# Performance work log

Hardware: AMD Instinct MI355X
Metric: run time of the kernel (lower is better)

Reference implementation:

```python
import jax, jax.numpy as jnp
import numpy as np

B, CTX, EMB = 4, 1024, 64
K, HID, NH = 8, 256, 8
GADD, NADD = 2, 2
RANK = 2                      # diags expand (..., k, 2) -> rank-2 index tuples
NPTS = K * (2 ** RANK + GADD + NADD)   # 64 points per token
SIGMA_BOOST = 2.0
EPS = 1e-6


def setup_inputs() -> dict:
    key = jax.random.key(0)
    ks = jax.random.split(key, 8)
    g = lambda k, shape, s: jax.random.normal(k, shape, jnp.float32) * s
    return {
        "x": g(ks[0], (B, CTX, EMB), 1.0),
        "Wq": g(ks[1], (EMB, EMB * NH), EMB ** -0.5),
        "Wk": g(ks[2], (EMB, EMB * NH), EMB ** -0.5),
        "Wv": g(ks[3], (EMB, EMB * NH), EMB ** -0.5),
        "Wu": g(ks[4], (EMB * NH, EMB), (EMB * NH) ** -0.5),
        "bu": jnp.zeros((EMB,), jnp.float32),
        "Wp1": g(ks[5], (EMB, HID), EMB ** -0.5),
        "bp1": jnp.zeros((HID,), jnp.float32),
        "Wp2": g(ks[6], (HID, 2 * K), HID ** -0.5),
        "bp2": jnp.zeros((2 * K,), jnp.float32),
        "mvalues": jnp.ones((CTX,), jnp.float32),
    }


def _forward(x, Wq, Wk, Wv, Wu, bu, Wp1, bp1, Wp2, bp2, mvalues):
    b, n, e = x.shape
    # ---- hyper network: per-token Gaussian mixture params ----
    h = jax.nn.relu(x @ Wp1 + bp1)
    params = h @ Wp2 + bp2                              # (b,n,2k)
    raw_means = params[:, :, :K][..., None]             # (b,n,k,1)
    raw_sigmas = params[:, :, K:]                       # (b,n,k)
    diags = jnp.arange(n, dtype=x.dtype)[None, :, None, None]
    means = jnp.broadcast_to(diags - jax.nn.softplus(raw_means), (b, n, K, RANK))
    means = jnp.clip(means, 0.0, n - 1.0)               # transform_means (clamp into range)
    sigmas = (jax.nn.softplus(raw_sigmas + SIGMA_BOOST) + EPS)[..., None]
    sigmas = jnp.broadcast_to(sigmas, (b, n, K, RANK))  # transform_sigmas

    # ---- ngenerate: 2^rank corners + global + local integer samples ----
    skey = jax.random.key(42)
    kg, kl = jax.random.split(skey)
    fl = jnp.floor(means).astype(jnp.int32)             # (b,n,k,2)
    offs = jnp.array([[0, 0], [0, 1], [1, 0], [1, 1]], jnp.int32)
    corners = fl[:, :, :, None, :] + offs               # (b,n,k,4,2)
    glob = jax.random.randint(kg, (b, n, K, GADD, RANK), 0, n)
    loc = fl[:, :, :, None, :] - 1 + jax.random.randint(kl, (b, n, K, NADD, RANK), 0, 2)
    idx = jnp.concatenate([corners, glob, loc], axis=3)
    idx = jnp.clip(idx, 0, n - 1).reshape(b, n, NPTS, RANK)

    # ---- nduplicates: mark repeat index tuples within each token ----
    eq = (idx[:, :, :, None, :] == idx[:, :, None, :, :]).all(-1)   # (b,n,p,p)
    tri = jnp.tril(jnp.ones((NPTS, NPTS), bool), -1)
    dup = (eq & tri).any(-1)                            # (b,n,p)

    # ---- densities: unnormalized Gaussians, zero dups, normalize over points ----
    pf = idx.astype(x.dtype)
    diff = (pf[:, :, :, None, :] - means[:, :, None, :, :]) / sigmas[:, :, None, :, :]
    dens = jnp.exp(-0.5 * (diff * diff).sum(-1))        # (b,n,p,k)
    dens = jnp.where(dup[..., None], 0.0, dens)
    dens = dens / dens.sum(axis=2, keepdims=True)
    weights = (mvalues[None, :, None, None] * dens).sum(-1)        # (b,n,p)

    # ---- heads ----
    BH = b * NH
    def heads(W):
        return (x @ W).reshape(b, n, NH, e).transpose(0, 2, 1, 3).reshape(BH, n, e)
    q = heads(Wq) / e ** 0.25
    k_ = heads(Wk) / e ** 0.25
    v = heads(Wv)

    P = n * NPTS
    idxh = jnp.broadcast_to(idx[:, None], (b, NH, n, NPTS, RANK)).reshape(BH, P, RANK)
    w = jnp.broadcast_to(weights[:, None], (b, NH, n, NPTS)).reshape(BH, P)
    rows, cols = idxh[..., 0], idxh[..., 1]

    # ---- gather q/k at sampled (row,col), per-element dot ----
    sq = jnp.take_along_axis(q, rows[:, :, None], axis=1)           # (BH,P,e)
    sk = jnp.take_along_axis(k_, cols[:, :, None], axis=1)
    dot = w * (sq * sk).sum(-1)                                     # (BH,P)

    # ---- sparse log-softmax over rows (stable, segment ops) ----
    seg = (jnp.arange(BH, dtype=jnp.int32)[:, None] * n + rows).reshape(-1)
    vflat = dot.reshape(-1)
    mx = jax.ops.segment_max(vflat, seg, num_segments=BH * n)
    ex = jnp.exp(vflat - mx[seg])
    Z = jax.ops.segment_sum(ex, seg, num_segments=BH * n)
    p = jnp.exp(vflat - (mx[seg] + jnp.log(Z[seg])))                # softmax probs

    # ---- sparse batchmm: scatter p * values[col] into rows ----
    sv = jnp.take_along_axis(v, cols[:, :, None], axis=1).reshape(-1, e)
    out = jax.ops.segment_sum(sv * p[:, None], seg, num_segments=BH * n)
    out = out.reshape(b, NH, n, e).transpose(0, 2, 1, 3).reshape(b, n, NH * e)
    return out @ Wu + bu


def reference(x, Wq, Wk, Wv, Wu, bu, Wp1, bp1, Wp2, bp2, mvalues):
    return _forward(x, Wq, Wk, Wv, Wu, bu, Wp1, bp1, Wp2, bp2, mvalues)
```

## Files before the change

kernel.cpp:

```cpp
#include <hip/hip_runtime.h>
#include <hip/hip_fp16.h>
#include <cstdint>
#include <cstddef>

#define BB 4
#define NN 1024
#define EMB_ 64
#define NH_ 8
#define BH_ (BB*NH_)
#define HID_ 256
#define K_ 8
#define NPTS_ 64
#define QB 512

__host__ __device__ inline void tf2x32(uint32_t k0, uint32_t k1, uint32_t c0, uint32_t c1,
                                       uint32_t &o0, uint32_t &o1) {
  uint32_t ks2 = k0 ^ k1 ^ 0x1BD11BDAu;
  uint32_t x0 = c0 + k0, x1 = c1 + k1;
#define TFR(r) { x0 += x1; x1 = (x1 << (r)) | (x1 >> (32 - (r))); x1 ^= x0; }
  TFR(13) TFR(15) TFR(26) TFR(6)
  x0 += k1;  x1 += ks2 + 1u;
  TFR(17) TFR(29) TFR(16) TFR(24)
  x0 += ks2; x1 += k0 + 2u;
  TFR(13) TFR(15) TFR(26) TFR(6)
  x0 += k0;  x1 += k1 + 3u;
  TFR(17) TFR(29) TFR(16) TFR(24)
  x0 += k1;  x1 += ks2 + 4u;
  TFR(13) TFR(15) TFR(26) TFR(6)
  x0 += ks2; x1 += k0 + 5u;
#undef TFR
  o0 = x0; o1 = x1;
}

__device__ inline uint32_t tf_bits(uint32_t k0, uint32_t k1, uint32_t idx) {
  uint32_t a, b;
  tf2x32(k0, k1, 0u, idx, a, b);
  return a ^ b;
}

__device__ inline float softplusf(float v) {
  return fmaxf(v, 0.f) + log1pf(expf(-fabsf(v)));
}

#define ROWS1 8
__global__ void __launch_bounds__(256) pre_kernel(
    const float* __restrict__ x,
    const float* __restrict__ Wq, const float* __restrict__ Wk, const float* __restrict__ Wv,
    const float* __restrict__ Wp1, const float* __restrict__ bp1,
    const float* __restrict__ Wp2, const float* __restrict__ bp2,
    const float* __restrict__ mvalues,
    float* __restrict__ q, __half* __restrict__ k, __half* __restrict__ v,
    int* __restrict__ prc, float* __restrict__ pw, int* __restrict__ counts,
    uint32_t kg0, uint32_t kg1, uint32_t kl0, uint32_t kl1) {
  __shared__ float xq[ROWS1][EMB_];
  __shared__ float xs[4][EMB_];
  __shared__ float hs[4][HID_];
  __shared__ float ps[4][16];
  __shared__ float meanv[4][K_], invsig[4][K_];
  __shared__ int flv[4][K_];
  __shared__ int pk[4][NPTS_];

  if (blockIdx.x < QB) {
    const int block0 = blockIdx.x * ROWS1;
    const int t = threadIdx.x;
    for (int i = t; i < ROWS1 * EMB_; i += 256) xq[i / EMB_][i % EMB_] = x[(size_t)block0 * EMB_ + i];
    __syncthreads();
    const float qkscale = 0.3535533905932738f;

    auto dmatf = [&](const float* __restrict__ W, float* __restrict__ o, float sc) {
      for (int half = 0; half < 2; half++) {
        const int c = half * 256 + t;
        float acc[ROWS1];
#pragma unroll
        for (int r = 0; r < ROWS1; r++) acc[r] = 0.f;
#pragma unroll 1
        for (int i4 = 0; i4 < EMB_; i4 += 4) {
          const float w0 = W[(i4 + 0) * 512 + c];
          const float w1 = W[(i4 + 1) * 512 + c];
          const float w2 = W[(i4 + 2) * 512 + c];
          const float w3 = W[(i4 + 3) * 512 + c];
#pragma unroll
          for (int r = 0; r < ROWS1; r++) {
            const float4 xv = *(const float4*)&xq[r][i4];
            acc[r] += xv.x * w0 + xv.y * w1 + xv.z * w2 + xv.w * w3;
          }
        }
        const int h = c >> 6, j = c & 63;
#pragma unroll
        for (int r = 0; r < ROWS1; r++) {
          const int gr = block0 + r;
          const int b = gr >> 10, n = gr & 1023;
          o[(((size_t)(b * NH_ + h) * NN + n)) * EMB_ + j] = acc[r] * sc;
        }
      }
    };
    auto dmath = [&](const float* __restrict__ W, __half* __restrict__ o, float sc) {
      for (int half = 0; half < 2; half++) {
        const int c = half * 256 + t;
        float acc[ROWS1];
#pragma unroll
        for (int r = 0; r < ROWS1; r++) acc[r] = 0.f;
#pragma unroll 1
        for (int i4 = 0; i4 < EMB_; i4 += 4) {
          const float w0 = W[(i4 + 0) * 512 + c];
          const float w1 = W[(i4 + 1) * 512 + c];
          const float w2 = W[(i4 + 2) * 512 + c];
          const float w3 = W[(i4 + 3) * 512 + c];
#pragma unroll
          for (int r = 0; r < ROWS1; r++) {
            const float4 xv = *(const float4*)&xq[r][i4];
            acc[r] += xv.x * w0 + xv.y * w1 + xv.z * w2 + xv.w * w3;
          }
        }
        const int h = c >> 6, j = c & 63;
#pragma unroll
        for (int r = 0; r < ROWS1; r++) {
          const int gr = block0 + r;
          const int b = gr >> 10, n = gr & 1023;
          o[(((size_t)(b * NH_ + h) * NN + n)) * EMB_ + j] = __float2half(acc[r] * sc);
        }
      }
    };
    dmatf(Wq, q, qkscale);
    dmath(Wk, k, qkscale);
    dmath(Wv, v, 1.0f);
    return;
  }

  const int w = threadIdx.x >> 6, lane = threadIdx.x & 63;
  const int bn = (blockIdx.x - QB) * 4 + w;
  const int b = bn >> 10, n = bn & 1023;

  xs[w][lane] = x[(size_t)bn * EMB_ + lane];
  __syncthreads();

#pragma unroll
  for (int cc = 0; cc < 4; cc++) {
    const int c = cc * 64 + lane;
    float a = bp1[c];
    for (int i = 0; i < EMB_; i++) a += xs[w][i] * Wp1[i * HID_ + c];
    hs[w][c] = fmaxf(a, 0.f);
  }
  __syncthreads();

  if (lane < 16) {
    float a = bp2[lane];
    for (int c = 0; c < HID_; c++) a += hs[w][c] * Wp2[c * 16 + lane];
    ps[w][lane] = a;
  }
  __syncthreads();

  if (lane < K_) {
    const float rm = ps[w][lane], rs = ps[w][K_ + lane];
    float mean = (float)n - softplusf(rm);
    mean = fminf(fmaxf(mean, 0.f), (float)(NN - 1));
    const float sig = softplusf(rs + 2.0f) + 1e-6f;
    meanv[w][lane] = mean;
    invsig[w][lane] = 1.f / sig;
    flv[w][lane] = (int)floorf(mean);
  }
  __syncthreads();

  const int kk = lane >> 3, j = lane & 7;
  const int fl = flv[w][kk];
  int row, col;
  if (j < 4) {
    row = fl + (j >> 1);
    col = fl + (j & 1);
  } else if (j < 6) {
    const int g = j - 4;
    const uint32_t base = ((uint32_t)(bn * K_ + kk) * 2u + (uint32_t)g) * 2u;
    row = (int)(tf_bits(kg0, kg1, base + 0u) & 1023u);
    col = (int)(tf_bits(kg0, kg1, base + 1u) & 1023u);
  } else {
    const int a = j - 6;
    const uint32_t base = ((uint32_t)(bn * K_ + kk) * 2u + (uint32_t)a) * 2u;
    row = fl - 1 + (int)(tf_bits(kl0, kl1, base + 0u) & 1u);
    col = fl - 1 + (int)(tf_bits(kl0, kl1, base + 1u) & 1u);
  }
  row = min(max(row, 0), NN - 1);
  col = min(max(col, 0), NN - 1);
  const int packed = (row << 16) | col;
  pk[w][lane] = packed;
  __syncthreads();

  bool dup = false;
  for (int p2 = 0; p2 < lane; p2++)
    if (pk[w][p2] == packed) dup = true;

  const float frow = (float)row, fcol = (float)col;
  float dens[K_];
#pragma unroll
  for (int qd = 0; qd < K_; qd++) {
    const float dx = (frow - meanv[w][qd]) * invsig[w][qd];
    const float dy = (fcol - meanv[w][qd]) * invsig[w][qd];
    dens[qd] = dup ? 0.f : expf(-0.5f * (dx * dx + dy * dy));
  }
  float wsum = 0.f;
#pragma unroll
  for (int qd = 0; qd < K_; qd++) {
    float s = dens[qd];
    for (int d = 1; d < 64; d <<= 1) s += __shfl_xor(s, d);
    wsum += dens[qd] / s;
  }
  const float wgt = mvalues[n] * wsum;

  prc[(size_t)bn * NPTS_ + lane] = packed;
  pw[(size_t)bn * NPTS_ + lane] = wgt;
  atomicAdd(&counts[b * NN + row], 1);
}

__global__ void __launch_bounds__(1024) scan_kernel(
    const int* __restrict__ counts,
    int* __restrict__ offs, int* __restrict__ cursor) {
  __shared__ int wsum[16];
  const int b = blockIdx.x, t = threadIdx.x;
  const int lane = t & 63, wid = t >> 6;
  const int vc = counts[b * NN + t];
  int vsc = vc;
#pragma unroll
  for (int d = 1; d < 64; d <<= 1) {
    const int up = __shfl_up(vsc, d);
    if (lane >= d) vsc += up;
  }
  if (lane == 63) wsum[wid] = vsc;
  __syncthreads();
  if (wid == 0 && lane < 16) {
    int s = wsum[lane];
#pragma unroll
    for (int d = 1; d < 16; d <<= 1) {
      const int up = __shfl_up(s, d);
      if (lane >= d) s += up;
    }
    wsum[lane] = s;
  }
  __syncthreads();
  const int excl = vsc + (wid > 0 ? wsum[wid - 1] : 0) - vc;
  offs[b * NN + t] = excl;
  cursor[b * NN + t] = excl;
}

__global__ void __launch_bounds__(256) scatter_kernel(
    const int* __restrict__ prc, const float* __restrict__ pw,
    int* __restrict__ cursor, uint32_t* __restrict__ scw) {
  const int e = blockIdx.x * 256 + threadIdx.x;
  const int b = e >> 16;
  const int pkt = prc[e];
  const int row = pkt >> 16;
  const uint32_t col = (uint32_t)(pkt & 0xFFFF);
  const uint32_t wbits = (uint32_t)__half_as_ushort(__float2half(pw[e]));
  const int pos = atomicAdd(&cursor[b * NN + row], 1);
  scw[((size_t)b << 16) + pos] = (col << 16) | wbits;
}

__global__ void __launch_bounds__(512) attn_out_kernel(
    const float* __restrict__ q, const __half* __restrict__ k, const __half* __restrict__ v,
    const int* __restrict__ offs, const int* __restrict__ counts,
    const uint32_t* __restrict__ scw,
    const float* __restrict__ Wu, const float* __restrict__ bu,
    float* __restrict__ out) {
  __shared__ float qs[NH_][EMB_];
  __shared__ float ps_lds[NH_][64];
  __shared__ int   cs_lds[NH_][64];
  __shared__ float ao[NH_][EMB_];
  __shared__ float op[NH_][EMB_];

  const int xcd = blockIdx.x & 7;
  const int rank = blockIdx.x >> 3;
  const int b = xcd >> 1;
  const int row = (rank << 1) | (xcd & 1);

  const int h = threadIdx.x >> 6, lane = threadIdx.x & 63;
  const int bh = b * NH_ + h;

  const __half* __restrict__ kb = k + (size_t)bh * NN * EMB_;
  const __half* __restrict__ vb = v + (size_t)bh * NN * EMB_;
  const uint32_t* __restrict__ sp = scw + ((size_t)b << 16);

  qs[h][lane] = q[((size_t)bh * NN + row) * EMB_ + lane];
  const int start = offs[b * NN + row];
  const int len = counts[b * NN + row];
  __syncthreads();

  float m = -INFINITY, Z = 0.f, acc = 0.f;

  for (int cb = 0; cb < len; cb += 64) {
    const int e = cb + lane;
    float logit = -INFINITY;
    int col = 0;
    if (e < len) {
      const uint32_t u = sp[start + e];
      col = (int)(u >> 16);
      const float wv = __half2float(__ushort_as_half((unsigned short)(u & 0xFFFFu)));
      const float4* __restrict__ kp4 = (const float4*)(kb + (size_t)col * EMB_);
      const float4* __restrict__ qp = (const float4*)qs[h];
      float dot = 0.f;
#pragma unroll
      for (int i = 0; i < 8; i++) {
        const float4 raw = kp4[i];
        const __half2* h2 = (const __half2*)&raw;
        const float4 qa = qp[i * 2];
        const float4 qb2 = qp[i * 2 + 1];
        const float2 f0 = __half22float2(h2[0]);
        const float2 f1 = __half22float2(h2[1]);
        const float2 f2 = __half22float2(h2[2]);
        const float2 f3 = __half22float2(h2[3]);
        dot += qa.x * f0.x + qa.y * f0.y + qa.z * f1.x + qa.w * f1.y;
        dot += qb2.x * f2.x + qb2.y * f2.y + qb2.z * f3.x + qb2.w * f3.y;
      }
      logit = wv * dot;
    }
    float cm = logit;
#pragma unroll
    for (int d = 1; d < 64; d <<= 1) cm = fmaxf(cm, __shfl_xor(cm, d));
    const float nm = fmaxf(m, cm);
    const float scale = expf(m - nm);
    const float p = expf(logit - nm);
    float zs = p;
#pragma unroll
    for (int d = 1; d < 64; d <<= 1) zs += __shfl_xor(zs, d);
    Z = Z * scale + zs;
    m = nm;

    ps_lds[h][lane] = p;
    cs_lds[h][lane] = col;

    acc *= scale;
    const int lim = len - cb;
#pragma unroll
    for (int g = 0; g < 8; g++) {
      if (g * 8 < lim) {
#pragma unroll
        for (int u8 = 0; u8 < 8; u8++) {
          const int ee = g * 8 + u8;
          acc += ps_lds[h][ee] * __half2float(vb[(size_t)cs_lds[h][ee] * EMB_ + lane]);
        }
      }
    }
  }

  ao[h][lane] = (len > 0) ? acc / Z : 0.f;
  __syncthreads();

  float s = 0.f;
  const float* __restrict__ wu_h = Wu + (size_t)(h * 64) * EMB_;
#pragma unroll
  for (int d = 0; d < 64; d++)
    s += ao[h][d] * wu_h[d * EMB_ + lane];
  op[h][lane] = s;
  __syncthreads();

  if (h == 0) {
    float t = bu[lane];
#pragma unroll
    for (int hh = 0; hh < NH_; hh++) t += op[hh][lane];
    out[(size_t)(b * NN + row) * EMB_ + lane] = t;
  }
}

extern "C" void kernel_launch(void* const* d_in, const int* in_sizes, int n_in,
                              void* d_out, int out_size, void* d_ws, size_t ws_size,
                              hipStream_t stream) {
  const float* x   = (const float*)d_in[0];
  const float* Wq  = (const float*)d_in[1];
  const float* Wk  = (const float*)d_in[2];
  const float* Wv  = (const float*)d_in[3];
  const float* Wu  = (const float*)d_in[4];
  const float* bu  = (const float*)d_in[5];
  const float* Wp1 = (const float*)d_in[6];
  const float* bp1 = (const float*)d_in[7];
  const float* Wp2 = (const float*)d_in[8];
  const float* bp2 = (const float*)d_in[9];
  const float* mv  = (const float*)d_in[10];
  float* out = (float*)d_out;

  char* ws = (char*)d_ws;
  size_t off = 0;
  auto alloc = [&](size_t bytes) -> void* {
    void* p = ws + off;
    off += (bytes + 255) & ~(size_t)255;
    return p;
  };
  const size_t QF = (size_t)BH_ * NN * EMB_ * sizeof(float);
  const size_t QH = (size_t)BH_ * NN * EMB_ * sizeof(__half);
  float*  q   = (float*) alloc(QF);
  __half* k   = (__half*)alloc(QH);
  __half* v   = (__half*)alloc(QH);
  int*   prc  = (int*)  alloc((size_t)BB * NN * NPTS_ * sizeof(int));
  float* pw   = (float*)alloc((size_t)BB * NN * NPTS_ * sizeof(float));
  int*   counts = (int*)alloc((size_t)BB * NN * sizeof(int));
  int*   offsA  = (int*)alloc((size_t)BB * NN * sizeof(int));
  int*   cursor = (int*)alloc((size_t)BB * NN * sizeof(int));
  uint32_t* scw = (uint32_t*)alloc((size_t)BB * NN * NPTS_ * sizeof(uint32_t));
  if (off > ws_size) return;

  uint32_t kgA, kgB, klA, klB;
  tf2x32(0u, 42u, 0u, 0u, kgA, kgB);
  tf2x32(0u, 42u, 0u, 1u, klA, klB);
  uint32_t kg2A, kg2B, kl2A, kl2B;
  tf2x32(kgA, kgB, 0u, 1u, kg2A, kg2B);
  tf2x32(klA, klB, 0u, 1u, kl2A, kl2B);

  hipMemsetAsync(counts, 0, (size_t)BB * NN * sizeof(int), stream);

  pre_kernel<<<QB + (BB * NN) / 4, 256, 0, stream>>>(
      x, Wq, Wk, Wv, Wp1, bp1, Wp2, bp2, mv, q, k, v, prc, pw, counts,
      kg2A, kg2B, kl2A, kl2B);
  scan_kernel<<<BB, 1024, 0, stream>>>(counts, offsA, cursor);
  scatter_kernel<<<(BB * NN * NPTS_) / 256, 256, 0, stream>>>(prc, pw, cursor, scw);
  attn_out_kernel<<<BB * NN, 512, 0, stream>>>(q, k, v, offsA, counts, scw,
                                               Wu, bu, out);
}
```

Measured before the change: 183.0 us.

## Replace count-scan-scatter with fixed-capacity per-row buckets filled by atomics

Instead of counting points per row, prefix-scanning, then scattering into a compact CSR array, the pre kernel appends each sampled point directly into a fixed-capacity (256) per-row bucket using an atomic cursor. This removes the scan and scatter kernel launches and the intermediate prc/pw buffers. The risk is silent truncation if any row receives more than 256 points, and a sparser, larger bucket array touched by the attention kernel.

```diff
diff --git a/kernel.cpp b/kernel.cpp
--- a/kernel.cpp
+++ b/kernel.cpp
@@ -12,6 +12,7 @@
 #define K_ 8
 #define NPTS_ 64
 #define QB 512
+#define CAP 256
 
 __host__ __device__ inline void tf2x32(uint32_t k0, uint32_t k1, uint32_t c0, uint32_t c1,
                                        uint32_t &o0, uint32_t &o1) {
@@ -50,7 +51,7 @@
     const float* __restrict__ Wp2, const float* __restrict__ bp2,
     const float* __restrict__ mvalues,
     float* __restrict__ q, __half* __restrict__ k, __half* __restrict__ v,
-    int* __restrict__ prc, float* __restrict__ pw, int* __restrict__ counts,
+    uint32_t* __restrict__ bucket, int* __restrict__ cursor,
     uint32_t kg0, uint32_t kg1, uint32_t kl0, uint32_t kl1) {
   __shared__ float xq[ROWS1][EMB_];
   __shared__ float xs[4][EMB_];
@@ -205,58 +206,16 @@
   }
   const float wgt = mvalues[n] * wsum;
 
-  prc[(size_t)bn * NPTS_ + lane] = packed;
-  pw[(size_t)bn * NPTS_ + lane] = wgt;
-  atomicAdd(&counts[b * NN + row], 1);
-}
-
-__global__ void __launch_bounds__(1024) scan_kernel(
-    const int* __restrict__ counts,
-    int* __restrict__ offs, int* __restrict__ cursor) {
-  __shared__ int wsum[16];
-  const int b = blockIdx.x, t = threadIdx.x;
-  const int lane = t & 63, wid = t >> 6;
-  const int vc = counts[b * NN + t];
-  int vsc = vc;
-#pragma unroll
-  for (int d = 1; d < 64; d <<= 1) {
-    const int up = __shfl_up(vsc, d);
-    if (lane >= d) vsc += up;
-  }
-  if (lane == 63) wsum[wid] = vsc;
-  __syncthreads();
-  if (wid == 0 && lane < 16) {
-    int s = wsum[lane];
-#pragma unroll
-    for (int d = 1; d < 16; d <<= 1) {
-      const int up = __shfl_up(s, d);
-      if (lane >= d) s += up;
-    }
-    wsum[lane] = s;
-  }
-  __syncthreads();
-  const int excl = vsc + (wid > 0 ? wsum[wid - 1] : 0) - vc;
-  offs[b * NN + t] = excl;
-  cursor[b * NN + t] = excl;
-}
-
-__global__ void __launch_bounds__(256) scatter_kernel(
-    const int* __restrict__ prc, const float* __restrict__ pw,
-    int* __restrict__ cursor, uint32_t* __restrict__ scw) {
-  const int e = blockIdx.x * 256 + threadIdx.x;
-  const int b = e >> 16;
-  const int pkt = prc[e];
-  const int row = pkt >> 16;
-  const uint32_t col = (uint32_t)(pkt & 0xFFFF);
-  const uint32_t wbits = (uint32_t)__half_as_ushort(__float2half(pw[e]));
-  const int pos = atomicAdd(&cursor[b * NN + row], 1);
-  scw[((size_t)b << 16) + pos] = (col << 16) | wbits;
+  const int seg = b * NN + row;
+  const uint32_t payload = ((uint32_t)col << 16) |
+                           (uint32_t)__half_as_ushort(__float2half(wgt));
+  const int pos = atomicAdd(&cursor[seg], 1);
+  if (pos < CAP) bucket[((size_t)seg << 8) + pos] = payload;
 }
 
 __global__ void __launch_bounds__(512) attn_out_kernel(
     const float* __restrict__ q, const __half* __restrict__ k, const __half* __restrict__ v,
-    const int* __restrict__ offs, const int* __restrict__ counts,
-    const uint32_t* __restrict__ scw,
+    const int* __restrict__ cursor, const uint32_t* __restrict__ bucket,
     const float* __restrict__ Wu, const float* __restrict__ bu,
     float* __restrict__ out) {
   __shared__ float qs[NH_][EMB_];
@@ -275,11 +234,11 @@
 
   const __half* __restrict__ kb = k + (size_t)bh * NN * EMB_;
   const __half* __restrict__ vb = v + (size_t)bh * NN * EMB_;
-  const uint32_t* __restrict__ sp = scw + ((size_t)b << 16);
+  const int seg = b * NN + row;
+  const uint32_t* __restrict__ sp = bucket + ((size_t)seg << 8);
 
   qs[h][lane] = q[((size_t)bh * NN + row) * EMB_ + lane];
-  const int start = offs[b * NN + row];
-  const int len = counts[b * NN + row];
+  const int len = min(cursor[seg], CAP);
   __syncthreads();
 
   float m = -INFINITY, Z = 0.f, acc = 0.f;
@@ -289,7 +248,7 @@
     float logit = -INFINITY;
     int col = 0;
     if (e < len) {
-      const uint32_t u = sp[start + e];
+      const uint32_t u = sp[e];
       col = (int)(u >> 16);
       const float wv = __half2float(__ushort_as_half((unsigned short)(u & 0xFFFFu)));
       const float4* __restrict__ kp4 = (const float4*)(kb + (size_t)col * EMB_);
@@ -383,15 +342,11 @@
   };
   const size_t QF = (size_t)BH_ * NN * EMB_ * sizeof(float);
   const size_t QH = (size_t)BH_ * NN * EMB_ * sizeof(__half);
-  float*  q   = (float*) alloc(QF);
-  __half* k   = (__half*)alloc(QH);
-  __half* v   = (__half*)alloc(QH);
-  int*   prc  = (int*)  alloc((size_t)BB * NN * NPTS_ * sizeof(int));
-  float* pw   = (float*)alloc((size_t)BB * NN * NPTS_ * sizeof(float));
-  int*   counts = (int*)alloc((size_t)BB * NN * sizeof(int));
-  int*   offsA  = (int*)alloc((size_t)BB * NN * sizeof(int));
-  int*   cursor = (int*)alloc((size_t)BB * NN * sizeof(int));
-  uint32_t* scw = (uint32_t*)alloc((size_t)BB * NN * NPTS_ * sizeof(uint32_t));
+  float*    q      = (float*)   alloc(QF);
+  __half*   k      = (__half*)  alloc(QH);
+  __half*   v      = (__half*)  alloc(QH);
+  uint32_t* bucket = (uint32_t*)alloc((size_t)BB * NN * CAP * sizeof(uint32_t));
+  int*      cursor = (int*)     alloc((size_t)BB * NN * sizeof(int));
   if (off > ws_size) return;
 
   uint32_t kgA, kgB, klA, klB;
@@ -401,13 +356,11 @@
   tf2x32(kgA, kgB, 0u, 1u, kg2A, kg2B);
   tf2x32(klA, klB, 0u, 1u, kl2A, kl2B);
 
-  hipMemsetAsync(counts, 0, (size_t)BB * NN * sizeof(int), stream);
+  hipMemsetAsync(cursor, 0, (size_t)BB * NN * sizeof(int), stream);
 
   pre_kernel<<<QB + (BB * NN) / 4, 256, 0, stream>>>(
-      x, Wq, Wk, Wv, Wp1, bp1, Wp2, bp2, mv, q, k, v, prc, pw, counts,
+      x, Wq, Wk, Wv, Wp1, bp1, Wp2, bp2, mv, q, k, v, bucket, cursor,
       kg2A, kg2B, kl2A, kl2B);
-  scan_kernel<<<BB, 1024, 0, stream>>>(counts, offsA, cursor);
-  scatter_kernel<<<(BB * NN * NPTS_) / 256, 256, 0, stream>>>(prc, pw, cursor, scw);
-  attn_out_kernel<<<BB * NN, 512, 0, stream>>>(q, k, v, offsA, counts, scw,
+  attn_out_kernel<<<BB * NN, 512, 0, stream>>>(q, k, v, cursor, bucket,
                                                Wu, bu, out);
 }
```

After: 209.0 us. +14.3%, slower.
